# Optimization experiments

Measured on AMD Instinct MI355X. Metric: run time of the kernel, lower is better.

The kernel has to match this reference:

```python
import jax, jax.numpy as jnp
import numpy as np

B, T, C, H, L, V = 64, 256, 256, 8, 6, 96
EPS = 1e-5


def _layernorm(x, w, b):
    m = x.mean(-1, keepdims=True)
    v = x.var(-1, keepdims=True)
    return (x - m) / jnp.sqrt(v + EPS) * w + b


def setup_inputs() -> dict:
    key = jax.random.key(0)
    ks = jax.random.split(key, 16)
    s = 0.05
    n = lambda k, sh: jax.random.normal(k, sh, jnp.float32) * s
    return {
        'idx': jax.random.randint(ks[0], (B, T), 0, V),
        'target': jax.random.randint(ks[1], (B, T), 0, V),
        'tok_emb': n(ks[2], (V, C)),
        'pos_emb': n(ks[3], (T, C)),
        'Wq': n(ks[4], (L, C, C)),
        'Wk': n(ks[5], (L, C, C)),
        'Wv': n(ks[6], (L, C, C)),
        'Wo': n(ks[7], (L, C, C)),
        'bo': jnp.zeros((L, C), jnp.float32),
        'W1': n(ks[8], (L, C, C)),
        'b1': jnp.zeros((L, C), jnp.float32),
        'W2': n(ks[9], (L, C, C)),
        'b2': jnp.zeros((L, C), jnp.float32),
        'ln1_w': jnp.ones((L, C), jnp.float32),
        'ln1_b': jnp.zeros((L, C), jnp.float32),
        'ln2_w': jnp.ones((L, C), jnp.float32),
        'ln2_b': jnp.zeros((L, C), jnp.float32),
        'lnf_w': jnp.ones((C,), jnp.float32),
        'lnf_b': jnp.zeros((C,), jnp.float32),
        'Wlm': n(ks[10], (C, V)),
        'blm': jnp.zeros((V,), jnp.float32),
    }


def _forward(idx, target, tok_emb, pos_emb, Wq, Wk, Wv, Wo, bo, W1, b1, W2, b2,
             ln1_w, ln1_b, ln2_w, ln2_b, lnf_w, lnf_b, Wlm, blm):
    Bc, Tc = idx.shape
    hs = C // H
    scale = C ** (-0.5)  # NOTE: original scales by n_embed**-0.5, not head_size**-0.5
    x = tok_emb[idx] + pos_emb[:Tc]              # [B,T,C]
    causal = jnp.tril(jnp.ones((Tc, Tc), bool))  # [T,T]
    for l in range(L):
        q = (x @ Wq[l]).reshape(Bc, Tc, H, hs)
        k = (x @ Wk[l]).reshape(Bc, Tc, H, hs)
        v = (x @ Wv[l]).reshape(Bc, Tc, H, hs)
        w = jnp.einsum('bqhd,bkhd->bhqk', q, k) * scale
        w = jnp.where(causal, w, -jnp.inf)
        w = jax.nn.softmax(w, axis=-1)
        att = jnp.einsum('bhqk,bkhd->bqhd', w, v).reshape(Bc, Tc, C)
        x = _layernorm(x + att @ Wo[l] + bo[l], ln1_w[l], ln1_b[l])  # post-residual LN
        h = jax.nn.relu(x @ W1[l] + b1[l]) @ W2[l] + b2[l]
        x = _layernorm(x + h, ln2_w[l], ln2_b[l])
    x = _layernorm(x, lnf_w, lnf_b)
    logits = (x @ Wlm + blm).reshape(Bc * Tc, V)
    logp = jax.nn.log_softmax(logits, axis=-1)
    nll = -jnp.take_along_axis(logp, target.reshape(-1, 1), axis=1)
    loss = nll.mean()
    return logits, loss


def reference(idx, target, tok_emb, pos_emb, Wq, Wk, Wv, Wo, bo, W1, b1, W2, b2,
              ln1_w, ln1_b, ln2_w, ln2_b, lnf_w, lnf_b, Wlm, blm):
    return _forward(idx, target, tok_emb, pos_emb, Wq, Wk, Wv, Wo, bo, W1, b1, W2, b2,
                    ln1_w, ln1_b, ln2_w, ln2_b, lnf_w, lnf_b, Wlm, blm)
```

## Files before the change

### kernel.cpp

```cpp
#include <hip/hip_runtime.h>

typedef unsigned short u16;

#define NT   16384
#define CDIM 256
#define LAYERS 6

using bf16x8 = __attribute__((ext_vector_type(8))) __bf16;
using f32x4  = __attribute__((ext_vector_type(4))) float;

__device__ __forceinline__ u16 f2bf(float x){
  unsigned u = __float_as_uint(x);
  u += 0x7fffu + ((u >> 16) & 1u);
  return (u16)(u >> 16);
}
__device__ __forceinline__ float bf2f(u16 u){
  return __uint_as_float(((unsigned)u) << 16);
}

__device__ __forceinline__ void gll16(const u16* g, u16* l){
  __builtin_amdgcn_global_load_lds(
      (const __attribute__((address_space(1))) unsigned int*)g,
      (__attribute__((address_space(3))) unsigned int*)l, 16, 0, 0);
}

__global__ __launch_bounds__(256) void wconv_k(
    const float* __restrict__ Wq, const float* __restrict__ Wk,
    const float* __restrict__ Wv, const float* __restrict__ Wo,
    const float* __restrict__ W1, const float* __restrict__ W2,
    const float* __restrict__ Wlm, u16* __restrict__ WT)
{
  __shared__ float tile[64][65];
  const int z = blockIdx.z;
  const float* src; u16* dst; int N = 256, Npad = 256;
  if (z < 18){
    const int l = z / 3, which = z % 3;
    const float* a[3] = {Wq, Wk, Wv};
    src = a[which] + (size_t)l * 65536;
    dst = WT + (size_t)l * 196608 + (size_t)which * 65536;
  } else if (z < 36){
    const int i = z - 18, j = i / 6, l = i % 6;
    const float* a[3] = {Wo, W1, W2};
    src = a[j] + (size_t)l * 65536;
    dst = WT + 1179648 + (size_t)(j * 6 + l) * 65536;
  } else {
    src = Wlm; dst = WT + 2359296; N = 96; Npad = 128;
  }
  const int n0 = blockIdx.y * 64, k0 = blockIdx.x * 64;
  if (n0 >= Npad) return;
  const int c = threadIdx.x & 63, r0 = threadIdx.x >> 6;
  #pragma unroll
  for (int i = 0; i < 16; ++i){
    const int r = r0 + i * 4;
    tile[r][c] = (n0 + c < N) ? src[(size_t)(k0 + r) * N + n0 + c] : 0.f;
  }
  __syncthreads();
  #pragma unroll
  for (int i = 0; i < 16; ++i){
    const int cp = r0 + i * 4;
    dst[(size_t)(n0 + cp) * CDIM + k0 + c] = f2bf(tile[c][cp]);
  }
}

__global__ __launch_bounds__(256) void embed_k(
    const int* __restrict__ idx, const float* __restrict__ tok,
    const float* __restrict__ pos, u16* __restrict__ X)
{
  const int w = threadIdx.x >> 6, l = threadIdx.x & 63;
  const int r = blockIdx.x * 4 + w;
  const int id = idx[r];
  float4 tv = *reinterpret_cast<const float4*>(tok + (size_t)id * CDIM + l * 4);
  float4 pv = *reinterpret_cast<const float4*>(pos + (size_t)(r & 255) * CDIM + l * 4);
  union { u16 u[4]; uint2 q; } p;
  p.u[0] = f2bf(tv.x + pv.x); p.u[1] = f2bf(tv.y + pv.y);
  p.u[2] = f2bf(tv.z + pv.z); p.u[3] = f2bf(tv.w + pv.w);
  *reinterpret_cast<uint2*>(X + (size_t)r * CDIM + l * 4) = p.q;
}

template<int TM, int TN, int WR, int WC, bool BIAS, bool RELU, bool RES, bool LN, bool F32OUT>
__global__ __launch_bounds__(WR * WC * 64) void gemm2_k(
    const u16* __restrict__ A, const u16* __restrict__ WT,
    const float* __restrict__ bias, const u16* __restrict__ res,
    void* __restrict__ outp, const float* __restrict__ lnw,
    const float* __restrict__ lnb, int N, int ldo)
{
  constexpr int THREADS = WR * WC * 64;
  constexpr int MR = TM / (WR * 16), NR = TN / (WC * 16);
  __shared__ u16 As[TM * 256];
  const int t = threadIdx.x, l = t & 63, w = t >> 6;
  const int wr = w / WC, wc = w % WC;
  const int m0 = blockIdx.x * TM, n0 = blockIdx.y * TN;
  const int lr = l & 15, lk = (l >> 4) * 8;
  const int rb = wr * (TM / WR), cb = wc * (TN / WC);
  f32x4 acc[MR][NR] = {};

  #pragma unroll
  for (int i = 0; i < TM * 32 / THREADS; ++i){
    const int eo = (i * THREADS + t) * 8;
    gll16(A + (size_t)(m0 + (eo >> 8)) * 256 + (eo & 255), As + eo);
  }
  __syncthreads();

  #pragma unroll
  for (int kk = 0; kk < 256; kk += 32){
    bf16x8 af[MR], bf[NR];
    #pragma unroll
    for (int m = 0; m < MR; ++m)
      af[m] = *reinterpret_cast<const bf16x8*>(&As[(rb + m * 16 + lr) * 256 + kk + lk]);
    #pragma unroll
    for (int n = 0; n < NR; ++n)
      bf[n] = *reinterpret_cast<const bf16x8*>(WT + (size_t)(n0 + cb + n * 16 + lr) * 256 + kk + lk);
    #pragma unroll
    for (int m = 0; m < MR; ++m)
      #pragma unroll
      for (int n = 0; n < NR; ++n)
        acc[m][n] = __builtin_amdgcn_mfma_f32_16x16x32_bf16(af[m], bf[n], acc[m][n], 0, 0, 0);
  }

  const int rj = (l >> 4) * 4;
  if constexpr (LN){
    __shared__ float redS[TM][WC + 1], redQ[TM][WC + 1];
    #pragma unroll
    for (int m = 0; m < MR; ++m){
      #pragma unroll
      for (int j = 0; j < 4; ++j){
        const int lrow = rb + m * 16 + rj + j;
        const int grow = m0 + lrow;
        float s = 0.f, q = 0.f;
        #pragma unroll
        for (int n = 0; n < NR; ++n){
          const int gcol = cb + n * 16 + lr;
          float v = acc[m][n][j] + bias[gcol] + bf2f(res[(size_t)grow * CDIM + gcol]);
          acc[m][n][j] = v;
          s += v; q += v * v;
        }
        #pragma unroll
        for (int o = 1; o < 16; o <<= 1){ s += __shfl_xor(s, o); q += __shfl_xor(q, o); }
        if (lr == 0){ redS[lrow][wc] = s; redQ[lrow][wc] = q; }
      }
    }
    __syncthreads();
    #pragma unroll
    for (int m = 0; m < MR; ++m){
      #pragma unroll
      for (int j = 0; j < 4; ++j){
        const int lrow = rb + m * 16 + rj + j;
        const int grow = m0 + lrow;
        float s = 0.f, q = 0.f;
        #pragma unroll
        for (int c = 0; c < WC; ++c){ s += redS[lrow][c]; q += redQ[lrow][c]; }
        const float mean = s * (1.f / 256.f);
        const float rstd = rsqrtf(q * (1.f / 256.f) - mean * mean + 1e-5f);
        #pragma unroll
        for (int n = 0; n < NR; ++n){
          const int gcol = cb + n * 16 + lr;
          const float y = (acc[m][n][j] - mean) * rstd * lnw[gcol] + lnb[gcol];
          ((u16*)outp)[(size_t)grow * CDIM + gcol] = f2bf(y);
        }
      }
    }
  } else {
    #pragma unroll
    for (int m = 0; m < MR; ++m){
      #pragma unroll
      for (int n = 0; n < NR; ++n){
        const int gcol = n0 + cb + n * 16 + lr;
        if (gcol < N){
          #pragma unroll
          for (int j = 0; j < 4; ++j){
            const int grow = m0 + rb + m * 16 + rj + j;
            const size_t o = (size_t)grow * ldo + gcol;
            float v = acc[m][n][j];
            if (BIAS) v += bias[gcol];
            if (RES)  v += bf2f(res[o]);
            if (RELU) v = fmaxf(v, 0.f);
            if (F32OUT) ((float*)outp)[o] = v;
            else        ((u16*)outp)[o] = f2bf(v);
          }
        }
      }
    }
  }
}

__global__ __launch_bounds__(256) void attn_k(
    const u16* __restrict__ QKV, u16* __restrict__ O)
{
  __shared__ u16 Vt[32][264];
  __shared__ u16 Ps[64][264];
  const int bh = blockIdx.x, b = bh >> 3, h = bh & 7;
  const size_t rbase = (size_t)b * 256 * 768;
  const int qc = h * 32, kc = 256 + h * 32, vc = 512 + h * 32;
  const int t = threadIdx.x, l = t & 63, w = t >> 6;
  const int lr = l & 15, lk = (l >> 4) * 8;

  {
    const uint4* vp = reinterpret_cast<const uint4*>(QKV + rbase + (size_t)t * 768 + vc);
    #pragma unroll
    for (int i = 0; i < 4; ++i){
      union { uint4 q; u16 u[8]; } p; p.q = vp[i];
      #pragma unroll
      for (int j = 0; j < 8; ++j) Vt[i * 8 + j][t] = p.u[j];
    }
  }
  bf16x8 kf[16];
  #pragma unroll
  for (int n = 0; n < 16; ++n)
    kf[n] = *reinterpret_cast<const bf16x8*>(QKV + rbase + (size_t)(n * 16 + lr) * 768 + kc + lk);
  __syncthreads();

  for (int c = 0; c < 4; ++c){
    const int rowb = c * 64 + w * 16;
    bf16x8 qa = *reinterpret_cast<const bf16x8*>(QKV + rbase + (size_t)(rowb + lr) * 768 + qc + lk);

    f32x4 s[16];
    #pragma unroll
    for (int n = 0; n < 16; ++n){
      f32x4 z = {};
      s[n] = __builtin_amdgcn_mfma_f32_16x16x32_bf16(qa, kf[n], z, 0, 0, 0);
    }

    float inv[4];
    const int prow = w * 16 + (l >> 4) * 4;
    #pragma unroll
    for (int j = 0; j < 4; ++j){
      const int qrow = rowb + (l >> 4) * 4 + j;
      float sv[16]; float mx = -1e30f;
      #pragma unroll
      for (int n = 0; n < 16; ++n){
        float vv = s[n][j] * 0.0625f;
        sv[n] = ((n * 16 + lr) <= qrow) ? vv : -1e30f;
        mx = fmaxf(mx, sv[n]);
      }
      #pragma unroll
      for (int o = 1; o < 16; o <<= 1) mx = fmaxf(mx, __shfl_xor(mx, o));
      float sum = 0.f;
      #pragma unroll
      for (int n = 0; n < 16; ++n){
        float p = __expf(sv[n] - mx);
        sum += p;
        Ps[prow + j][n * 16 + lr] = f2bf(p);
      }
      #pragma unroll
      for (int o = 1; o < 16; o <<= 1) sum += __shfl_xor(sum, o);
      inv[j] = 1.f / sum;
    }
    __syncthreads();

    f32x4 o0 = {}, o1 = {};
    #pragma unroll
    for (int kc2 = 0; kc2 < 8; ++kc2){
      bf16x8 pa = *reinterpret_cast<const bf16x8*>(&Ps[w * 16 + lr][kc2 * 32 + lk]);
      bf16x8 v0 = *reinterpret_cast<const bf16x8*>(&Vt[lr][kc2 * 32 + lk]);
      bf16x8 v1 = *reinterpret_cast<const bf16x8*>(&Vt[16 + lr][kc2 * 32 + lk]);
      o0 = __builtin_amdgcn_mfma_f32_16x16x32_bf16(pa, v0, o0, 0, 0, 0);
      o1 = __builtin_amdgcn_mfma_f32_16x16x32_bf16(pa, v1, o1, 0, 0, 0);
    }
    #pragma unroll
    for (int j = 0; j < 4; ++j){
      const int qrow = rowb + (l >> 4) * 4 + j;
      u16* op = O + (size_t)(b * 256 + qrow) * CDIM + h * 32;
      op[lr]      = f2bf(o0[j] * inv[j]);
      op[16 + lr] = f2bf(o1[j] * inv[j]);
    }
    __syncthreads();
  }
}

__global__ __launch_bounds__(256) void lnf_k(
    const u16* __restrict__ in, const float* __restrict__ w,
    const float* __restrict__ b, u16* __restrict__ out)
{
  const int wv = threadIdx.x >> 6, l = threadIdx.x & 63;
  const int r = blockIdx.x * 4 + wv;
  union { uint2 q; u16 u[4]; } iv;
  iv.q = *reinterpret_cast<const uint2*>(in + (size_t)r * CDIM + l * 4);
  float v0 = bf2f(iv.u[0]), v1 = bf2f(iv.u[1]), v2 = bf2f(iv.u[2]), v3 = bf2f(iv.u[3]);
  float s = v0 + v1 + v2 + v3;
  float q = v0 * v0 + v1 * v1 + v2 * v2 + v3 * v3;
  #pragma unroll
  for (int o = 32; o; o >>= 1){ s += __shfl_xor(s, o); q += __shfl_xor(q, o); }
  const float mean = s * (1.f / 256.f);
  const float rstd = rsqrtf(q * (1.f / 256.f) - mean * mean + 1e-5f);
  float4 w4 = *reinterpret_cast<const float4*>(w + l * 4);
  float4 b4 = *reinterpret_cast<const float4*>(b + l * 4);
  union { u16 u[4]; uint2 q2; } p;
  p.u[0] = f2bf((v0 - mean) * rstd * w4.x + b4.x);
  p.u[1] = f2bf((v1 - mean) * rstd * w4.y + b4.y);
  p.u[2] = f2bf((v2 - mean) * rstd * w4.z + b4.z);
  p.u[3] = f2bf((v3 - mean) * rstd * w4.w + b4.w);
  *reinterpret_cast<uint2*>(out + (size_t)r * CDIM + l * 4) = p.q2;
}

__global__ __launch_bounds__(256) void nll_k(
    const float* __restrict__ logits, const int* __restrict__ target,
    float* __restrict__ nll)
{
  const int w = threadIdx.x >> 6, l = threadIdx.x & 63;
  const int r = blockIdx.x * 4 + w;
  const float* row = logits + (size_t)r * 96;
  float v0 = row[l];
  float v1 = (l < 32) ? row[64 + l] : -1e30f;
  float m = fmaxf(v0, v1);
  #pragma unroll
  for (int o = 32; o; o >>= 1) m = fmaxf(m, __shfl_xor(m, o));
  float s = __expf(v0 - m) + ((l < 32) ? __expf(v1 - m) : 0.f);
  #pragma unroll
  for (int o = 32; o; o >>= 1) s += __shfl_xor(s, o);
  if (l == 0) nll[r] = logf(s) + m - row[target[r]];
}

__global__ __launch_bounds__(256) void loss_k(
    const float* __restrict__ nll, float* __restrict__ out)
{
  __shared__ float rs[4];
  float s = 0.f;
  for (int i = threadIdx.x; i < NT; i += 256) s += nll[i];
  #pragma unroll
  for (int o = 32; o; o >>= 1) s += __shfl_xor(s, o);
  if ((threadIdx.x & 63) == 0) rs[threadIdx.x >> 6] = s;
  __syncthreads();
  if (threadIdx.x == 0) out[0] = (rs[0] + rs[1] + rs[2] + rs[3]) * (1.f / 16384.f);
}

extern "C" void kernel_launch(void* const* d_in, const int* in_sizes, int n_in,
                              void* d_out, int out_size, void* d_ws, size_t ws_size,
                              hipStream_t stream)
{
  const int*   idx    = (const int*)  d_in[0];
  const int*   target = (const int*)  d_in[1];
  const float* tok    = (const float*)d_in[2];
  const float* pos    = (const float*)d_in[3];
  const float* Wq     = (const float*)d_in[4];
  const float* Wk     = (const float*)d_in[5];
  const float* Wv     = (const float*)d_in[6];
  const float* Wo     = (const float*)d_in[7];
  const float* bo     = (const float*)d_in[8];
  const float* W1     = (const float*)d_in[9];
  const float* b1     = (const float*)d_in[10];
  const float* W2     = (const float*)d_in[11];
  const float* b2     = (const float*)d_in[12];
  const float* ln1w   = (const float*)d_in[13];
  const float* ln1b   = (const float*)d_in[14];
  const float* ln2w   = (const float*)d_in[15];
  const float* ln2b   = (const float*)d_in[16];
  const float* lnfw   = (const float*)d_in[17];
  const float* lnfb   = (const float*)d_in[18];
  const float* blm    = (const float*)d_in[20];
  float* out = (float*)d_out;

  char* ws = (char*)d_ws;
  u16*   X   = (u16*)  (ws);
  u16*   QKV = (u16*)  (ws + ( 8u << 20));
  u16*   O   = (u16*)  (ws + (32u << 20));
  u16*   hB  = (u16*)  (ws + (40u << 20));
  u16*   Xf  = (u16*)  (ws + (48u << 20));
  u16*   WT  = (u16*)  (ws + (56u << 20));
  float* nl  = (float*)(ws + (64u << 20));

  wconv_k<<<dim3(4, 4, 37), 256, 0, stream>>>(Wq, Wk, Wv, Wo, W1, W2,
                                              (const float*)d_in[19], WT);
  embed_k<<<NT / 4, 256, 0, stream>>>(idx, tok, pos, X);

  for (int l = 0; l < LAYERS; ++l){
    const u16* wqkv = WT + (size_t)l * 196608;
    const u16* wo   = WT + 1179648 + (size_t)(0 * 6 + l) * 65536;
    const u16* w1   = WT + 1179648 + (size_t)(1 * 6 + l) * 65536;
    const u16* w2   = WT + 1179648 + (size_t)(2 * 6 + l) * 65536;

    gemm2_k<128, 128, 2, 4, false, false, false, false, false>
        <<<dim3(128, 6), 512, 0, stream>>>(
        X, wqkv, nullptr, nullptr, QKV, nullptr, nullptr, 768, 768);
    attn_k<<<512, 256, 0, stream>>>(QKV, O);
    gemm2_k<64, 256, 2, 4, true, false, true, true, false>
        <<<dim3(256, 1), 512, 0, stream>>>(
        O, wo, bo + l * 256, X, X, ln1w + l * 256, ln1b + l * 256, 256, 256);
    gemm2_k<64, 128, 2, 4, true, true, false, false, false>
        <<<dim3(256, 2), 512, 0, stream>>>(
        X, w1, b1 + l * 256, nullptr, hB, nullptr, nullptr, 256, 256);
    gemm2_k<64, 256, 2, 4, true, false, true, true, false>
        <<<dim3(256, 1), 512, 0, stream>>>(
        hB, w2, b2 + l * 256, X, X, ln2w + l * 256, ln2b + l * 256, 256, 256);
  }

  lnf_k<<<NT / 4, 256, 0, stream>>>(X, lnfw, lnfb, Xf);
  gemm2_k<64, 128, 2, 4, true, false, false, false, true>
      <<<dim3(256, 1), 512, 0, stream>>>(
      Xf, WT + 2359296, blm, nullptr, out, nullptr, nullptr, 96, 96);
  nll_k<<<NT / 4, 256, 0, stream>>>(out, target, nl);
  loss_k<<<1, 256, 0, stream>>>(nl, out + (size_t)NT * 96);
}
```

Measured before the change: 684.3 us.

## Double-buffer GEMM K-tiles in LDS and skip masked causal blocks in attention

The GEMM kernel now stages both A and weight tiles in 64-wide K chunks into double-buffered shared memory via global_load_lds, overlapping the next tile's load with the current tile's MFMAs instead of reading weights straight from global memory. The LayerNorm-fused GEMMs use 1024 threads with 8 column waves. Attention stages K and Q through padded shared memory and skips QK^T and PV MFMAs for key blocks fully above the causal diagonal. This adds barriers per K step and more dynamic shared memory, which may lower occupancy.

Measured after the change: 620.4 us. 1.1x faster.

```diff
diff --git a/kernel.cpp b/kernel.cpp
--- a/kernel.cpp
+++ b/kernel.cpp
@@ -3,11 +3,12 @@
 typedef unsigned short u16;
 
 #define NT   16384
-#define CDIM 256
 #define LAYERS 6
 
 using bf16x8 = __attribute__((ext_vector_type(8))) __bf16;
 using f32x4  = __attribute__((ext_vector_type(4))) float;
+
+#define MFMA __builtin_amdgcn_mfma_f32_16x16x32_bf16
 
 __device__ __forceinline__ u16 f2bf(float x){
   unsigned u = __float_as_uint(x);
@@ -58,7 +59,7 @@
   #pragma unroll
   for (int i = 0; i < 16; ++i){
     const int cp = r0 + i * 4;
-    dst[(size_t)(n0 + cp) * CDIM + k0 + c] = f2bf(tile[c][cp]);
+    dst[(size_t)(n0 + cp) * 256 + k0 + c] = f2bf(tile[c][cp]);
   }
 }
 
@@ -69,74 +70,98 @@
   const int w = threadIdx.x >> 6, l = threadIdx.x & 63;
   const int r = blockIdx.x * 4 + w;
   const int id = idx[r];
-  float4 tv = *reinterpret_cast<const float4*>(tok + (size_t)id * CDIM + l * 4);
-  float4 pv = *reinterpret_cast<const float4*>(pos + (size_t)(r & 255) * CDIM + l * 4);
+  float4 tv = *reinterpret_cast<const float4*>(tok + (size_t)id * 256 + l * 4);
+  float4 pv = *reinterpret_cast<const float4*>(pos + (size_t)(r & 255) * 256 + l * 4);
   union { u16 u[4]; uint2 q; } p;
   p.u[0] = f2bf(tv.x + pv.x); p.u[1] = f2bf(tv.y + pv.y);
   p.u[2] = f2bf(tv.z + pv.z); p.u[3] = f2bf(tv.w + pv.w);
-  *reinterpret_cast<uint2*>(X + (size_t)r * CDIM + l * 4) = p.q;
-}
-
-template<int TM, int TN, int WR, int WC, bool BIAS, bool RELU, bool RES, bool LN, bool F32OUT>
-__global__ __launch_bounds__(WR * WC * 64) void gemm2_k(
+  *reinterpret_cast<uint2*>(X + (size_t)r * 256 + l * 4) = p.q;
+}
+
+template<int TM, int TN, int THREADS, int WR, int WC,
+         bool BIAS, bool RELU, bool RES, bool LN, bool F32OUT>
+__global__ __launch_bounds__(THREADS) void gemm3_k(
     const u16* __restrict__ A, const u16* __restrict__ WT,
     const float* __restrict__ bias, const u16* __restrict__ res,
     void* __restrict__ outp, const float* __restrict__ lnw,
     const float* __restrict__ lnb, int N, int ldo)
 {
-  constexpr int THREADS = WR * WC * 64;
   constexpr int MR = TM / (WR * 16), NR = TN / (WC * 16);
-  __shared__ u16 As[TM * 256];
+  extern __shared__ char smem[];
+  u16* As = (u16*)smem;
+  u16* Bs = As + 2 * TM * 64;
+  float* redS = (float*)(Bs + 2 * TN * 64);
+  float* redQ = redS + TM * (WC + 1);
+
   const int t = threadIdx.x, l = t & 63, w = t >> 6;
   const int wr = w / WC, wc = w % WC;
   const int m0 = blockIdx.x * TM, n0 = blockIdx.y * TN;
-  const int lr = l & 15, lk = (l >> 4) * 8;
+  const int lr = l & 15, lk = (l >> 4) * 8, rj = (l >> 4) * 4;
   const int rb = wr * (TM / WR), cb = wc * (TN / WC);
   f32x4 acc[MR][NR] = {};
 
-  #pragma unroll
-  for (int i = 0; i < TM * 32 / THREADS; ++i){
-    const int eo = (i * THREADS + t) * 8;
-    gll16(A + (size_t)(m0 + (eo >> 8)) * 256 + (eo & 255), As + eo);
-  }
+  auto stage = [&](int buf, int kt){
+    const int k0 = kt * 64;
+    u16* as = As + buf * (TM * 64);
+    u16* bs = Bs + buf * (TN * 64);
+    #pragma unroll
+    for (int ci = t; ci < TM * 8; ci += THREADS){
+      const int eo = ci * 8;
+      gll16(A + (size_t)(m0 + (eo >> 6)) * 256 + k0 + (eo & 63), as + eo);
+    }
+    #pragma unroll
+    for (int ci = t; ci < TN * 8; ci += THREADS){
+      const int eo = ci * 8;
+      gll16(WT + (size_t)(n0 + (eo >> 6)) * 256 + k0 + (eo & 63), bs + eo);
+    }
+  };
+  auto compute = [&](int buf){
+    const u16* as = As + buf * (TM * 64);
+    const u16* bs = Bs + buf * (TN * 64);
+    #pragma unroll
+    for (int kk = 0; kk < 64; kk += 32){
+      bf16x8 af[MR], bf[NR];
+      #pragma unroll
+      for (int m = 0; m < MR; ++m)
+        af[m] = *reinterpret_cast<const bf16x8*>(&as[(rb + m*16 + lr) * 64 + kk + lk]);
+      #pragma unroll
+      for (int n = 0; n < NR; ++n)
+        bf[n] = *reinterpret_cast<const bf16x8*>(&bs[(cb + n*16 + lr) * 64 + kk + lk]);
+      #pragma unroll
+      for (int m = 0; m < MR; ++m)
+        #pragma unroll
+        for (int n = 0; n < NR; ++n)
+          acc[m][n] = MFMA(af[m], bf[n], acc[m][n], 0, 0, 0);
+    }
+  };
+
+  stage(0, 0);
   __syncthreads();
-
-  #pragma unroll
-  for (int kk = 0; kk < 256; kk += 32){
-    bf16x8 af[MR], bf[NR];
-    #pragma unroll
-    for (int m = 0; m < MR; ++m)
-      af[m] = *reinterpret_cast<const bf16x8*>(&As[(rb + m * 16 + lr) * 256 + kk + lk]);
-    #pragma unroll
-    for (int n = 0; n < NR; ++n)
-      bf[n] = *reinterpret_cast<const bf16x8*>(WT + (size_t)(n0 + cb + n * 16 + lr) * 256 + kk + lk);
-    #pragma unroll
-    for (int m = 0; m < MR; ++m)
-      #pragma unroll
-      for (int n = 0; n < NR; ++n)
-        acc[m][n] = __builtin_amdgcn_mfma_f32_16x16x32_bf16(af[m], bf[n], acc[m][n], 0, 0, 0);
-  }
-
-  const int rj = (l >> 4) * 4;
+  #pragma unroll
+  for (int kt = 0; kt < 4; ++kt){
+    if (kt < 3) stage((kt + 1) & 1, kt + 1);
+    compute(kt & 1);
+    if (kt < 3) __syncthreads();
+  }
+
   if constexpr (LN){
-    __shared__ float redS[TM][WC + 1], redQ[TM][WC + 1];
     #pragma unroll
     for (int m = 0; m < MR; ++m){
       #pragma unroll
       for (int j = 0; j < 4; ++j){
-        const int lrow = rb + m * 16 + rj + j;
+        const int lrow = rb + m*16 + rj + j;
         const int grow = m0 + lrow;
         float s = 0.f, q = 0.f;
         #pragma unroll
         for (int n = 0; n < NR; ++n){
-          const int gcol = cb + n * 16 + lr;
-          float v = acc[m][n][j] + bias[gcol] + bf2f(res[(size_t)grow * CDIM + gcol]);
+          const int gcol = cb + n*16 + lr;
+          float v = acc[m][n][j] + bias[gcol] + bf2f(res[(size_t)grow * 256 + gcol]);
           acc[m][n][j] = v;
           s += v; q += v * v;
         }
         #pragma unroll
         for (int o = 1; o < 16; o <<= 1){ s += __shfl_xor(s, o); q += __shfl_xor(q, o); }
-        if (lr == 0){ redS[lrow][wc] = s; redQ[lrow][wc] = q; }
+        if (lr == 0){ redS[lrow*(WC+1) + wc] = s; redQ[lrow*(WC+1) + wc] = q; }
       }
     }
     __syncthreads();
@@ -144,18 +169,18 @@
     for (int m = 0; m < MR; ++m){
       #pragma unroll
       for (int j = 0; j < 4; ++j){
-        const int lrow = rb + m * 16 + rj + j;
+        const int lrow = rb + m*16 + rj + j;
         const int grow = m0 + lrow;
         float s = 0.f, q = 0.f;
         #pragma unroll
-        for (int c = 0; c < WC; ++c){ s += redS[lrow][c]; q += redQ[lrow][c]; }
-        const float mean = s * (1.f / 256.f);
-        const float rstd = rsqrtf(q * (1.f / 256.f) - mean * mean + 1e-5f);
+        for (int c = 0; c < WC; ++c){ s += redS[lrow*(WC+1) + c]; q += redQ[lrow*(WC+1) + c]; }
+        const float mean = s * (1.f/256.f);
+        const float rstd = rsqrtf(q * (1.f/256.f) - mean*mean + 1e-5f);
         #pragma unroll
         for (int n = 0; n < NR; ++n){
-          const int gcol = cb + n * 16 + lr;
-          const float y = (acc[m][n][j] - mean) * rstd * lnw[gcol] + lnb[gcol];
-          ((u16*)outp)[(size_t)grow * CDIM + gcol] = f2bf(y);
+          const int gcol = cb + n*16 + lr;
+          ((u16*)outp)[(size_t)grow * 256 + gcol] =
+              f2bf((acc[m][n][j] - mean) * rstd * lnw[gcol] + lnb[gcol]);
         }
       }
     }
@@ -164,11 +189,11 @@
     for (int m = 0; m < MR; ++m){
       #pragma unroll
       for (int n = 0; n < NR; ++n){
-        const int gcol = n0 + cb + n * 16 + lr;
+        const int gcol = n0 + cb + n*16 + lr;
         if (gcol < N){
           #pragma unroll
           for (int j = 0; j < 4; ++j){
-            const int grow = m0 + rb + m * 16 + rj + j;
+            const int grow = m0 + rb + m*16 + rj + j;
             const size_t o = (size_t)grow * ldo + gcol;
             float v = acc[m][n][j];
             if (BIAS) v += bias[gcol];
@@ -183,63 +208,76 @@
   }
 }
 
-__global__ __launch_bounds__(256) void attn_k(
+__global__ __launch_bounds__(256) void attn2_k(
     const u16* __restrict__ QKV, u16* __restrict__ O)
 {
-  __shared__ u16 Vt[32][264];
-  __shared__ u16 Ps[64][264];
+  extern __shared__ char smem[];
+  u16* Ks = (u16*)smem;
+  u16* Qs = Ks + 256 * 40;
+  u16* VT = Qs + 64 * 40;
+  u16* Ps = VT + 32 * 264;
+
   const int bh = blockIdx.x, b = bh >> 3, h = bh & 7;
   const size_t rbase = (size_t)b * 256 * 768;
   const int qc = h * 32, kc = 256 + h * 32, vc = 512 + h * 32;
   const int t = threadIdx.x, l = t & 63, w = t >> 6;
-  const int lr = l & 15, lk = (l >> 4) * 8;
-
-  {
-    const uint4* vp = reinterpret_cast<const uint4*>(QKV + rbase + (size_t)t * 768 + vc);
-    #pragma unroll
-    for (int i = 0; i < 4; ++i){
-      union { uint4 q; u16 u[8]; } p; p.q = vp[i];
-      #pragma unroll
-      for (int j = 0; j < 8; ++j) Vt[i * 8 + j][t] = p.u[j];
-    }
-  }
+  const int lr = l & 15, lk = (l >> 4) * 8, rj = (l >> 4) * 4;
+  const int r4 = t >> 2, c8 = (t & 3) * 8;
+
+  #pragma unroll
+  for (int it = 0; it < 4; ++it){
+    const int row = it * 64 + r4;
+    *reinterpret_cast<uint4*>(Ks + row * 40 + c8) =
+        *reinterpret_cast<const uint4*>(QKV + rbase + (size_t)row * 768 + kc + c8);
+    union { uint4 q; u16 u[8]; } p;
+    p.q = *reinterpret_cast<const uint4*>(QKV + rbase + (size_t)row * 768 + vc + c8);
+    #pragma unroll
+    for (int j2 = 0; j2 < 8; ++j2) VT[(c8 + j2) * 264 + row] = p.u[j2];
+  }
+  __syncthreads();
+
   bf16x8 kf[16];
   #pragma unroll
   for (int n = 0; n < 16; ++n)
-    kf[n] = *reinterpret_cast<const bf16x8*>(QKV + rbase + (size_t)(n * 16 + lr) * 768 + kc + lk);
-  __syncthreads();
-
+    kf[n] = *reinterpret_cast<const bf16x8*>(Ks + (n*16 + lr) * 40 + lk);
+
+  #pragma unroll 1
   for (int c = 0; c < 4; ++c){
-    const int rowb = c * 64 + w * 16;
-    bf16x8 qa = *reinterpret_cast<const bf16x8*>(QKV + rbase + (size_t)(rowb + lr) * 768 + qc + lk);
-
+    *reinterpret_cast<uint4*>(Qs + r4 * 40 + c8) =
+        *reinterpret_cast<const uint4*>(QKV + rbase + (size_t)(c*64 + r4) * 768 + qc + c8);
+    __syncthreads();
+
+    bf16x8 qa = *reinterpret_cast<const bf16x8*>(Qs + (w*16 + lr) * 40 + lk);
+    const int nmax = 4 * (c + 1);
     f32x4 s[16];
     #pragma unroll
     for (int n = 0; n < 16; ++n){
-      f32x4 z = {};
-      s[n] = __builtin_amdgcn_mfma_f32_16x16x32_bf16(qa, kf[n], z, 0, 0, 0);
-    }
-
+      if (n < nmax){ f32x4 z = {}; s[n] = MFMA(qa, kf[n], z, 0, 0, 0); }
+    }
     float inv[4];
-    const int prow = w * 16 + (l >> 4) * 4;
     #pragma unroll
     for (int j = 0; j < 4; ++j){
-      const int qrow = rowb + (l >> 4) * 4 + j;
-      float sv[16]; float mx = -1e30f;
+      const int tq = c*64 + w*16 + rj + j;
+      float m = -1e30f;
       #pragma unroll
       for (int n = 0; n < 16; ++n){
-        float vv = s[n][j] * 0.0625f;
-        sv[n] = ((n * 16 + lr) <= qrow) ? vv : -1e30f;
-        mx = fmaxf(mx, sv[n]);
-      }
-      #pragma unroll
-      for (int o = 1; o < 16; o <<= 1) mx = fmaxf(mx, __shfl_xor(mx, o));
+        if (n < nmax){
+          float v = s[n][j] * 0.0625f;
+          v = ((n*16 + lr) <= tq) ? v : -1e30f;
+          s[n][j] = v;
+          m = fmaxf(m, v);
+        }
+      }
+      #pragma unroll
+      for (int o = 1; o < 16; o <<= 1) m = fmaxf(m, __shfl_xor(m, o));
       float sum = 0.f;
       #pragma unroll
       for (int n = 0; n < 16; ++n){
-        float p = __expf(sv[n] - mx);
-        sum += p;
-        Ps[prow + j][n * 16 + lr] = f2bf(p);
+        if (n < nmax){
+          const float p = __expf(s[n][j] - m);
+          sum += p;
+          Ps[(w*16 + rj + j) * 264 + n*16 + lr] = f2bf(p);
+        }
       }
       #pragma unroll
       for (int o = 1; o < 16; o <<= 1) sum += __shfl_xor(sum, o);
@@ -249,17 +287,19 @@
 
     f32x4 o0 = {}, o1 = {};
     #pragma unroll
-    for (int kc2 = 0; kc2 < 8; ++kc2){
-      bf16x8 pa = *reinterpret_cast<const bf16x8*>(&Ps[w * 16 + lr][kc2 * 32 + lk]);
-      bf16x8 v0 = *reinterpret_cast<const bf16x8*>(&Vt[lr][kc2 * 32 + lk]);
-      bf16x8 v1 = *reinterpret_cast<const bf16x8*>(&Vt[16 + lr][kc2 * 32 + lk]);
-      o0 = __builtin_amdgcn_mfma_f32_16x16x32_bf16(pa, v0, o0, 0, 0, 0);
-      o1 = __builtin_amdgcn_mfma_f32_16x16x32_bf16(pa, v1, o1, 0, 0, 0);
+    for (int k2 = 0; k2 < 8; ++k2){
+      if (k2 < 2 * (c + 1)){
+        bf16x8 pa  = *reinterpret_cast<const bf16x8*>(Ps + (w*16 + lr) * 264 + k2*32 + lk);
+        bf16x8 vb0 = *reinterpret_cast<const bf16x8*>(VT + lr * 264 + k2*32 + lk);
+        bf16x8 vb1 = *reinterpret_cast<const bf16x8*>(VT + (16 + lr) * 264 + k2*32 + lk);
+        o0 = MFMA(pa, vb0, o0, 0, 0, 0);
+        o1 = MFMA(pa, vb1, o1, 0, 0, 0);
+      }
     }
     #pragma unroll
     for (int j = 0; j < 4; ++j){
-      const int qrow = rowb + (l >> 4) * 4 + j;
-      u16* op = O + (size_t)(b * 256 + qrow) * CDIM + h * 32;
+      const int row = c*64 + w*16 + rj + j;
+      u16* op = O + (size_t)(b*256 + row) * 256 + h*32;
       op[lr]      = f2bf(o0[j] * inv[j]);
       op[16 + lr] = f2bf(o1[j] * inv[j]);
     }
@@ -274,14 +314,14 @@
   const int wv = threadIdx.x >> 6, l = threadIdx.x & 63;
   const int r = blockIdx.x * 4 + wv;
   union { uint2 q; u16 u[4]; } iv;
-  iv.q = *reinterpret_cast<const uint2*>(in + (size_t)r * CDIM + l * 4);
+  iv.q = *reinterpret_cast<const uint2*>(in + (size_t)r * 256 + l * 4);
   float v0 = bf2f(iv.u[0]), v1 = bf2f(iv.u[1]), v2 = bf2f(iv.u[2]), v3 = bf2f(iv.u[3]);
   float s = v0 + v1 + v2 + v3;
-  float q = v0 * v0 + v1 * v1 + v2 * v2 + v3 * v3;
+  float q = v0*v0 + v1*v1 + v2*v2 + v3*v3;
   #pragma unroll
   for (int o = 32; o; o >>= 1){ s += __shfl_xor(s, o); q += __shfl_xor(q, o); }
-  const float mean = s * (1.f / 256.f);
-  const float rstd = rsqrtf(q * (1.f / 256.f) - mean * mean + 1e-5f);
+  const float mean = s * (1.f/256.f);
+  const float rstd = rsqrtf(q * (1.f/256.f) - mean*mean + 1e-5f);
   float4 w4 = *reinterpret_cast<const float4*>(w + l * 4);
   float4 b4 = *reinterpret_cast<const float4*>(b + l * 4);
   union { u16 u[4]; uint2 q2; } p;
@@ -289,7 +329,7 @@
   p.u[1] = f2bf((v1 - mean) * rstd * w4.y + b4.y);
   p.u[2] = f2bf((v2 - mean) * rstd * w4.z + b4.z);
   p.u[3] = f2bf((v3 - mean) * rstd * w4.w + b4.w);
-  *reinterpret_cast<uint2*>(out + (size_t)r * CDIM + l * 4) = p.q2;
+  *reinterpret_cast<uint2*>(out + (size_t)r * 256 + l * 4) = p.q2;
 }
 
 __global__ __launch_bounds__(256) void nll_k(
@@ -331,14 +371,8 @@
   const int*   target = (const int*)  d_in[1];
   const float* tok    = (const float*)d_in[2];
   const float* pos    = (const float*)d_in[3];
-  const float* Wq     = (const float*)d_in[4];
-  const float* Wk     = (const float*)d_in[5];
-  const float* Wv     = (const float*)d_in[6];
-  const float* Wo     = (const float*)d_in[7];
   const float* bo     = (const float*)d_in[8];
-  const float* W1     = (const float*)d_in[9];
   const float* b1     = (const float*)d_in[10];
-  const float* W2     = (const float*)d_in[11];
   const float* b2     = (const float*)d_in[12];
   const float* ln1w   = (const float*)d_in[13];
   const float* ln1b   = (const float*)d_in[14];
@@ -350,42 +384,49 @@
   float* out = (float*)d_out;
 
   char* ws = (char*)d_ws;
-  u16*   X   = (u16*)  (ws);
-  u16*   QKV = (u16*)  (ws + ( 8u << 20));
-  u16*   O   = (u16*)  (ws + (32u << 20));
-  u16*   hB  = (u16*)  (ws + (40u << 20));
-  u16*   Xf  = (u16*)  (ws + (48u << 20));
-  u16*   WT  = (u16*)  (ws + (56u << 20));
-  float* nl  = (float*)(ws + (64u << 20));
-
-  wconv_k<<<dim3(4, 4, 37), 256, 0, stream>>>(Wq, Wk, Wv, Wo, W1, W2,
-                                              (const float*)d_in[19], WT);
+  u16*   X   = (u16*)(ws);
+  u16*   QKV = (u16*)(ws + ( 8u << 20));
+  u16*   O   = (u16*)(ws + (32u << 20));
+  u16*   hB  = (u16*)(ws + (40u << 20));
+  u16*   Xf  = (u16*)(ws + (48u << 20));
+  u16*   WT  = (u16*)(ws + (56u << 20));
+  float* nl  = (float*)(ws + (62u << 20));
+
+  const size_t SM_QKV = (size_t)2*(128+128)*64*2 + 2*128*5*4;
+  const size_t SM_LN  = (size_t)2*(64+256)*64*2 + 2*64*9*4;
+  const size_t SM_W1  = (size_t)2*(64+128)*64*2 + 2*64*5*4;
+  const size_t SM_AT  = (size_t)(256*40 + 64*40 + 32*264 + 64*264) * 2;
+
+  wconv_k<<<dim3(4, 4, 37), 256, 0, stream>>>(
+      (const float*)d_in[4], (const float*)d_in[5], (const float*)d_in[6],
+      (const float*)d_in[7], (const float*)d_in[9], (const float*)d_in[11],
+      (const float*)d_in[19], WT);
   embed_k<<<NT / 4, 256, 0, stream>>>(idx, tok, pos, X);
 
   for (int l = 0; l < LAYERS; ++l){
     const u16* wqkv = WT + (size_t)l * 196608;
-    const u16* wo   = WT + 1179648 + (size_t)(0 * 6 + l) * 65536;
-    const u16* w1   = WT + 1179648 + (size_t)(1 * 6 + l) * 65536;
-    const u16* w2   = WT + 1179648 + (size_t)(2 * 6 + l) * 65536;
-
-    gemm2_k<128, 128, 2, 4, false, false, false, false, false>
-        <<<dim3(128, 6), 512, 0, stream>>>(
+    const u16* wo   = WT + 1179648 + (size_t)(0*6 + l) * 65536;
+    const u16* w1   = WT + 1179648 + (size_t)(1*6 + l) * 65536;
+    const u16* w2   = WT + 1179648 + (size_t)(2*6 + l) * 65536;
+
+    gemm3_k<128,128,512,2,4, false,false,false,false,false>
+        <<<dim3(128, 6), 512, SM_QKV, stream>>>(
         X, wqkv, nullptr, nullptr, QKV, nullptr, nullptr, 768, 768);
-    attn_k<<<512, 256, 0, stream>>>(QKV, O);
-    gemm2_k<64, 256, 2, 4, true, false, true, true, false>
-        <<<dim3(256, 1), 512, 0, stream>>>(
-        O, wo, bo + l * 256, X, X, ln1w + l * 256, ln1b + l * 256, 256, 256);
-    gemm2_k<64, 128, 2, 4, true, true, false, false, false>
-        <<<dim3(256, 2), 512, 0, stream>>>(
-        X, w1, b1 + l * 256, nullptr, hB, nullptr, nullptr, 256, 256);
-    gemm2_k<64, 256, 2, 4, true, false, true, true, false>
-        <<<dim3(256, 1), 512, 0, stream>>>(
-        hB, w2, b2 + l * 256, X, X, ln2w + l * 256, ln2b + l * 256, 256, 256);
+    attn2_k<<<512, 256, SM_AT, stream>>>(QKV, O);
+    gemm3_k<64,256,1024,2,8, true,false,true,true,false>
+        <<<dim3(256, 1), 1024, SM_LN, stream>>>(
+        O, wo, bo + l*256, X, X, ln1w + l*256, ln1b + l*256, 256, 256);
+    gemm3_k<64,128,512,2,4, true,true,false,false,false>
+        <<<dim3(256, 2), 512, SM_W1, stream>>>(
+        X, w1, b1 + l*256, nullptr, hB, nullptr, nullptr, 256, 256);
+    gemm3_k<64,256,1024,2,8, true,false,true,true,false>
+        <<<dim3(256, 1), 1024, SM_LN, stream>>>(
+        hB, w2, b2 + l*256, X, X, ln2w + l*256, ln2b + l*256, 256, 256);
   }
 
   lnf_k<<<NT / 4, 256, 0, stream>>>(X, lnfw, lnfb, Xf);
-  gemm2_k<64, 128, 2, 4, true, false, false, false, true>
-      <<<dim3(256, 1), 512, 0, stream>>>(
+  gemm3_k<64,128,512,2,4, true,false,false,false,true>
+      <<<dim3(256, 1), 512, SM_W1, stream>>>(
       Xf, WT + 2359296, blm, nullptr, out, nullptr, nullptr, 96, 96);
   nll_k<<<NT / 4, 256, 0, stream>>>(out, target, nl);
   loss_k<<<1, 256, 0, stream>>>(nl, out + (size_t)NT * 96);
```
